# Kernel tuning notes

Measured on AMD Instinct MI355X. Metric: run time of the kernel, lower is better.

Reference implementation:

```python
import jax, jax.numpy as jnp
import numpy as np

# Poincare ball, curvature c = 1. Assumed manifold ops (standard hyperbolic-attention
# formulations, matching the hypll-style API used by the module):
#   HLinear(x)                ~ expmap0(logmap0(x) @ W + b)   (tangent-space linear)
#   attention_similarity      ~ (-d_poincare(q,k))/tau + gamma
#   attention_activation      ~ softmax over keys
#   attention_midpoint        ~ Mobius gyromidpoint: 0.5 (x) [sum_k w lam(v) v / sum_k w (lam(v)-1)]
#   cat                       ~ expmap0(concat(logmap0(heads)))

EPS = 1e-6
MAX_TANH_ARG = 1.0 - 1e-5

def _norm(x):
    return jnp.sqrt(jnp.clip(jnp.sum(x * x, axis=-1, keepdims=True), EPS))

def expmap0(v):
    n = _norm(v)
    return jnp.tanh(n) * v / n

def logmap0(x):
    n = _norm(x)
    return jnp.arctanh(jnp.minimum(n, MAX_TANH_ARG)) * x / n

def hlinear(x, W, b):
    return expmap0(logmap0(x) @ W + b)

def pairwise_poincare_dist(q, k):
    # q: [B,H,Sq,D] on ball, k: [B,Sk,D] on ball -> d: [B,H,Sq,Sk]
    qn = jnp.clip(jnp.sum(q * q, axis=-1), 0.0, 1.0 - 1e-5)            # [B,H,Sq]
    kn = jnp.clip(jnp.sum(k * k, axis=-1), 0.0, 1.0 - 1e-5)            # [B,Sk]
    dot = jnp.einsum('bhqd,bkd->bhqk', q, k)                            # GEMM-like
    sq = jnp.clip(qn[..., :, None] + kn[:, None, None, :] - 2.0 * dot, 0.0)
    denom = jnp.clip((1.0 - qn)[..., :, None] * (1.0 - kn)[:, None, None, :], EPS)
    arg = 1.0 + 2.0 * sq / denom
    return jnp.arccosh(jnp.maximum(arg, 1.0 + 1e-7))

def mobius_scalar_mul(r, x):
    n = _norm(x)
    return jnp.tanh(r * jnp.arctanh(jnp.minimum(n, MAX_TANH_ARG))) * x / n


def reference(query, key, value, Wq, bq, Wk, bk, Wv, bv, Wo, bo, scale_tau, scale_gamma):
    # batch_first=True; query/key/value: [B,S,D] points on the Poincare ball
    B, S, D = query.shape
    H = Wq.shape[0]

    # per-head full-dimension query projections, vectorized over heads
    tq = logmap0(query)                                                 # [B,S,D]
    q_h = expmap0(jnp.einsum('bsd,hde->bhse', tq, Wq) + bq[None, :, None, :])  # [B,H,S,D]
    # shared K/V projections (use_separate_kv_per_head=False -> MQA)
    k = hlinear(key, Wk, bk)                                            # [B,S,D]
    v = hlinear(value, Wv, bv)                                          # [B,S,D]

    tau = jnp.exp(-scale_tau[0])          # module passes tau = 1/exp(scale_tau)
    gamma = scale_gamma[0]

    d = pairwise_poincare_dist(q_h, k)                                  # [B,H,Sq,Sk]
    sim = -d / tau + gamma
    w = jax.nn.softmax(sim, axis=-1)                                    # [B,H,Sq,Sk]

    # Mobius gyromidpoint of values, weighted per query
    vn = jnp.clip(jnp.sum(v * v, axis=-1), 0.0, 1.0 - 1e-5)             # [B,Sk]
    lam = 2.0 / (1.0 - vn)                                              # [B,Sk]
    num = jnp.einsum('bhqk,bk,bkd->bhqd', w, lam, v)                    # [B,H,Sq,D]
    den = jnp.einsum('bhqk,bk->bhq', w, lam - 1.0)[..., None]           # [B,H,Sq,1]
    mid = mobius_scalar_mul(0.5, num / jnp.clip(den, EPS))              # [B,H,Sq,D]

    # manifold.cat: tangent-space concat of heads, back to the ball
    t = logmap0(mid)                                                    # [B,H,S,D]
    t = jnp.transpose(t, (0, 2, 1, 3)).reshape(B, S, H * D)             # [B,S,H*D]
    concat = expmap0(t)
    return hlinear(concat, Wo, bo)                                      # [B,S,D]


def setup_inputs() -> dict:
    key0 = jax.random.key(0)
    ks = jax.random.split(key0, 16)
    B, S, D, H = 4, 1024, 512, 8
    proj = lambda k: expmap0(0.02 * jax.random.normal(k, (B, S, D), dtype=jnp.float32))
    w_init = lambda k, shape, fan_in: (jax.random.normal(k, shape, dtype=jnp.float32) / np.sqrt(fan_in)).astype(jnp.float32)
    return {
        'query': proj(ks[0]),
        'key': proj(ks[1]),
        'value': proj(ks[2]),
        'Wq': w_init(ks[3], (H, D, D), D),
        'bq': 0.01 * jax.random.normal(ks[4], (H, D), dtype=jnp.float32),
        'Wk': w_init(ks[5], (D, D), D),
        'bk': 0.01 * jax.random.normal(ks[6], (D,), dtype=jnp.float32),
        'Wv': w_init(ks[7], (D, D), D),
        'bv': 0.01 * jax.random.normal(ks[8], (D,), dtype=jnp.float32),
        'Wo': w_init(ks[9], (H * D, D), H * D),
        'bo': 0.01 * jax.random.normal(ks[10], (D,), dtype=jnp.float32),
        'scale_tau': jnp.zeros((1,), dtype=jnp.float32),
        'scale_gamma': jnp.zeros((1,), dtype=jnp.float32),
    }
```

## Files before the change

kernel.cpp:

```cpp
#include <hip/hip_runtime.h>
#include <math.h>

constexpr int B_ = 4, S_ = 1024, D_ = 512, H_ = 8;
constexpr float EPS_ = 1e-6f;
constexpr float MAXT = 1.0f - 1e-5f;

typedef __attribute__((ext_vector_type(8))) short bf16x8;
typedef __attribute__((ext_vector_type(4))) float f32x4;

__device__ __forceinline__ ushort f2b(float f) {
    unsigned u = __float_as_uint(f);
    unsigned r = u + 0x7fffu + ((u >> 16) & 1u);
    return (ushort)(r >> 16);
}
__device__ __forceinline__ float b2f(ushort h) {
    return __uint_as_float(((unsigned)h) << 16);
}

__device__ __forceinline__ void async16(const ushort* g, ushort* l) {
    __builtin_amdgcn_global_load_lds(
        (const __attribute__((address_space(1))) unsigned int*)g,
        (__attribute__((address_space(3))) unsigned int*)l, 16, 0, 0);
}

__device__ __forceinline__ float blk_reduce_sum(float v, float* sm) {
    for (int o = 32; o > 0; o >>= 1) v += __shfl_down(v, o, 64);
    int lane = threadIdx.x & 63, wid = threadIdx.x >> 6;
    if (lane == 0) sm[wid] = v;
    __syncthreads();
    if (threadIdx.x == 0) sm[0] = sm[0] + sm[1] + sm[2] + sm[3];
    __syncthreads();
    float r = sm[0];
    __syncthreads();
    return r;
}

constexpr int GC_ABUF = 256 * 32;
constexpr int GC_BUF = (256 + 128) * 32;
constexpr int GC_SH = GC_BUF * 3;

__device__ __forceinline__ void gemm_core256(const ushort* __restrict__ A,
                                             const ushort* __restrict__ B,
                                             int lda, int ldb, int K, int m0, int n0,
                                             ushort* __restrict__ sh, f32x4 acc[4][8]) {
    const int tid = threadIdx.x;
    const int w = tid >> 6, lane = tid & 63;
    const int quad = lane >> 4, lx = lane & 15;
    const int rr = lane >> 2, c = lane & 3;

    const ushort* aP[4];
    int aOff[4];
#pragma unroll
    for (int i = 0; i < 4; i++) {
        int r = w * 64 + i * 16 + rr;
        int q = c ^ ((r >> 1) & 3);
        aP[i] = A + (size_t)(m0 + r) * lda + q * 8;
        aOff[i] = (w * 64 + i * 16) * 32;
    }
    const ushort* bP[2];
    int bOff[2];
#pragma unroll
    for (int i = 0; i < 2; i++) {
        int r = w * 32 + i * 16 + rr;
        int q = c ^ ((r >> 1) & 3);
        bP[i] = B + (size_t)(n0 + r) * ldb + q * 8;
        bOff[i] = GC_ABUF + (w * 32 + i * 16) * 32;
    }

    int raOff[4], rbOff[8];
#pragma unroll
    for (int i = 0; i < 4; i++) {
        int ra = w * 64 + i * 16 + lx;
        raOff[i] = ra * 32 + (quad ^ ((ra >> 1) & 3)) * 8;
    }
#pragma unroll
    for (int j = 0; j < 8; j++) {
        int rb = j * 16 + lx;
        rbOff[j] = GC_ABUF + rb * 32 + (quad ^ ((rb >> 1) & 3)) * 8;
    }
#pragma unroll
    for (int i = 0; i < 4; i++)
#pragma unroll
        for (int j = 0; j < 8; j++) acc[i][j] = (f32x4)(0.0f);

    const int nsteps = K >> 5;
#pragma unroll
    for (int i = 0; i < 4; i++) async16(aP[i], sh + aOff[i]);
#pragma unroll
    for (int i = 0; i < 2; i++) async16(bP[i], sh + bOff[i]);
#pragma unroll
    for (int i = 0; i < 4; i++) async16(aP[i] + 32, sh + GC_BUF + aOff[i]);
#pragma unroll
    for (int i = 0; i < 2; i++) async16(bP[i] + 32, sh + GC_BUF + bOff[i]);

    int bufid = 0;
    for (int s = 0; s < nsteps; s++) {
        ushort* cur = sh + bufid * GC_BUF;
        if (s + 2 < nsteps) {
            int nb = bufid + 2;
            if (nb >= 3) nb -= 3;
            ushort* nxt = sh + nb * GC_BUF;
            int k0 = (s + 2) << 5;
#pragma unroll
            for (int i = 0; i < 4; i++) async16(aP[i] + k0, nxt + aOff[i]);
#pragma unroll
            for (int i = 0; i < 2; i++) async16(bP[i] + k0, nxt + bOff[i]);
            asm volatile("s_waitcnt vmcnt(12)" ::: "memory");
        } else if (s + 1 < nsteps) {
            asm volatile("s_waitcnt vmcnt(6)" ::: "memory");
        } else {
            asm volatile("s_waitcnt vmcnt(0)" ::: "memory");
        }
        asm volatile("s_barrier" ::: "memory");
        bf16x8 af[4], bfr[8];
#pragma unroll
        for (int i = 0; i < 4; i++) af[i] = *(const bf16x8*)(cur + raOff[i]);
#pragma unroll
        for (int j = 0; j < 8; j++) bfr[j] = *(const bf16x8*)(cur + rbOff[j]);
#pragma unroll
        for (int i = 0; i < 4; i++)
#pragma unroll
            for (int j = 0; j < 8; j++)
                acc[i][j] = __builtin_amdgcn_mfma_f32_16x16x32_bf16(af[i], bfr[j], acc[i][j], 0, 0, 0);
        asm volatile("s_waitcnt lgkmcnt(0)" ::: "memory");
        asm volatile("s_barrier" ::: "memory");
        bufid = (bufid == 2) ? 0 : bufid + 1;
    }
}

__global__ __launch_bounds__(256, 2) void k_gemm_proj_all(const ushort* __restrict__ tq,
                                                          const ushort* __restrict__ tk,
                                                          const ushort* __restrict__ tv,
                                                          const ushort* __restrict__ WqT,
                                                          const ushort* __restrict__ WkT,
                                                          const ushort* __restrict__ WvT,
                                                          const float* __restrict__ bq,
                                                          const float* __restrict__ bk,
                                                          const float* __restrict__ bv,
                                                          ushort* __restrict__ yq,
                                                          ushort* __restrict__ yk,
                                                          ushort* __restrict__ yv,
                                                          float* __restrict__ ssq,
                                                          float* __restrict__ ssk,
                                                          float* __restrict__ ssv) {
    __shared__ ushort sh[GC_SH];
    int z = blockIdx.z;
    const ushort* A;
    const ushort* BT;
    const float* bias;
    ushort* C;
    float* SS;
    int remap = 0, h = 0;
    if (z == 0) { A = tk; BT = WkT; bias = bk; C = yk; SS = ssk; }
    else if (z == 1) { A = tv; BT = WvT; bias = bv; C = yv; SS = ssv; }
    else {
        h = z - 2;
        A = tq; BT = WqT + (size_t)h * 512 * 512; bias = bq + (size_t)h * 512;
        C = yq; SS = ssq; remap = 1;
    }
    f32x4 acc[4][8];
    int m0 = blockIdx.y * 256, n0 = blockIdx.x * 128;
    gemm_core256(A, BT, 512, 512, 512, m0, n0, sh, acc);
    int tid = threadIdx.x, w = tid >> 6, lane = tid & 63;
    int quad = lane >> 4, lx = lane & 15;
#pragma unroll
    for (int i = 0; i < 4; i++)
#pragma unroll
        for (int reg = 0; reg < 4; reg++) {
            int m = m0 + w * 64 + i * 16 + quad * 4 + reg;
            size_t orow = remap ? (size_t)((m >> 10) * H_ + h) * S_ + (m & 1023) : (size_t)m;
            float ssum = 0.0f;
#pragma unroll
            for (int j = 0; j < 8; j++) {
                int n = n0 + j * 16 + lx;
                ushort hb = f2b(acc[i][j][reg] + bias[n]);
                C[orow * 512 + n] = hb;
                float yv_ = b2f(hb);
                ssum += yv_ * yv_;
            }
            for (int o = 8; o; o >>= 1) ssum += __shfl_xor(ssum, o, 64);
            if (lx == 0) atomicAdd(&SS[orow], ssum);
        }
}

__global__ __launch_bounds__(256) void k_post_proj(const ushort* __restrict__ yv,
                                                   ushort* __restrict__ yvT,
                                                   const float* __restrict__ ssq,
                                                   const float* __restrict__ ssk,
                                                   const float* __restrict__ ssv,
                                                   float* __restrict__ fq,
                                                   float* __restrict__ qn2,
                                                   float* __restrict__ fk,
                                                   float* __restrict__ kn2,
                                                   float* __restrict__ cv,
                                                   float* __restrict__ dsc) {
    int lin = blockIdx.x;
    if (lin < 2048) {
        __shared__ ushort t[32][34];
        int z = lin >> 9, rem = lin & 511;
        int by = rem >> 4, bx = rem & 15;
        const ushort* in = yv + (size_t)z * 1024 * 512;
        ushort* out = yvT + (size_t)z * 512 * 1024;
        int c0 = bx * 32, r0 = by * 32;
        int tx = threadIdx.x & 31, ty = threadIdx.x >> 5;
        for (int rr = ty; rr < 32; rr += 8) t[rr][tx] = in[(size_t)(r0 + rr) * 512 + c0 + tx];
        __syncthreads();
        for (int rr = ty; rr < 32; rr += 8)
            out[(size_t)(c0 + rr) * 1024 + r0 + tx] = t[tx][rr];
        return;
    }
    int idx = (lin - 2048) * 256 + threadIdx.x;
    if (idx >= 40960) return;
    float ss;
    if (idx < 32768) ss = ssq[idx];
    else if (idx < 36864) ss = ssk[idx - 32768];
    else ss = ssv[idx - 36864];
    float n = sqrtf(fmaxf(ss, EPS_));
    float f = tanhf(n) / n;
    float bn2 = fminf(f * f * ss, MAXT);
    if (idx < 32768) {
        fq[idx] = f;
        qn2[idx] = bn2;
    } else if (idx < 36864) {
        fk[idx - 32768] = f;
        kn2[idx - 32768] = bn2;
    } else {
        int r = idx - 36864;
        float lam = 2.0f / (1.0f - bn2);
        float c = f * lam;
        cv[r] = c;
        dsc[r] = (lam - 1.0f) / c;
    }
}

__global__ __launch_bounds__(256, 2) void k_gemm_score(const ushort* __restrict__ Yq,
                                                       const ushort* __restrict__ Yk,
                                                       ushort* __restrict__ E,
                                                       float* __restrict__ den,
                                                       const float* __restrict__ fq,
                                                       const float* __restrict__ qn2,
                                                       const float* __restrict__ fk,
                                                       const float* __restrict__ kn2,
                                                       const float* __restrict__ cv,
                                                       const float* __restrict__ dsc,
                                                       const float* __restrict__ stau) {
    __shared__ ushort sh[GC_SH];
    int b = blockIdx.z;
    int m0 = blockIdx.y * 256, n0 = blockIdx.x * 128;
    const ushort* Aq = Yq + (size_t)b * 8192 * 512;
    const ushort* Bk = Yk + (size_t)b * 1024 * 512;
    E += (size_t)b * 8192 * 1024;
    den += (size_t)b * 8192;
    const float* fqb = fq + (size_t)b * 8192;
    const float* qn2b = qn2 + (size_t)b * 8192;
    const float* fkb = fk + (size_t)b * 1024;
    const float* kn2b = kn2 + (size_t)b * 1024;
    const float* cvb = cv + (size_t)b * 1024;
    const float* dscb = dsc + (size_t)b * 1024;

    f32x4 acc[4][8];
    gemm_core256(Aq, Bk, 512, 512, 512, m0, n0, sh, acc);
    float itau = expf(stau[0]);
    bool tau1 = (itau == 1.0f);
    int tid = threadIdx.x, w_ = tid >> 6, lane = tid & 63;
    int quad = lane >> 4, lx = lane & 15;
    float fkv[8], kn2v[8], cvv[8], dscv[8], rk[8];
#pragma unroll
    for (int j = 0; j < 8; j++) {
        int n = n0 + j * 16 + lx;
        fkv[j] = fkb[n];
        kn2v[j] = kn2b[n];
        rk[j] = __builtin_amdgcn_rcpf(1.0f - kn2v[j]);
        cvv[j] = cvb[n];
        dscv[j] = dscb[n];
    }
#pragma unroll
    for (int i = 0; i < 4; i++)
#pragma unroll
        for (int reg = 0; reg < 4; reg++) {
            int m = m0 + w_ * 64 + i * 16 + quad * 4 + reg;
            float fqm = fqb[m];
            float q = qn2b[m];
            float rq2 = 2.0f * __builtin_amdgcn_rcpf(1.0f - q);
            float rsum = 0.0f;
#pragma unroll
            for (int j = 0; j < 8; j++) {
                float dot = fqm * fkv[j] * acc[i][j][reg];
                float sq = fmaxf(q + kn2v[j] - 2.0f * dot, 0.0f);
                float rr2 = fminf(rq2 * rk[j], 2e6f);
                float w = fmaxf(sq * rr2, 1e-7f);
                float root = __builtin_amdgcn_sqrtf(__builtin_fmaf(w, w, 2.0f * w));
                float t = 1.0f + w + root;
                float e = tau1 ? __builtin_amdgcn_rcpf(t)
                               : __builtin_amdgcn_exp2f(-itau * __builtin_amdgcn_logf(t));
                ushort eb = f2b(e * cvv[j]);
                int n = n0 + j * 16 + lx;
                E[(size_t)m * 1024 + n] = eb;
                rsum += b2f(eb) * dscv[j];
            }
            for (int o = 8; o; o >>= 1) rsum += __shfl_xor(rsum, o, 64);
            if (lx == 0) atomicAdd(&den[m], rsum);
        }
}

__global__ __launch_bounds__(256, 2) void k_gemm_attnv(const ushort* __restrict__ E,
                                                       const ushort* __restrict__ VT,
                                                       const float* __restrict__ den,
                                                       ushort* __restrict__ Ub,
                                                       float* __restrict__ ssU) {
    __shared__ ushort sh[GC_SH];
    int b = blockIdx.z;
    int m0 = blockIdx.y * 256, n0 = blockIdx.x * 128;
    E += (size_t)b * 8192 * 1024;
    VT += (size_t)b * 512 * 1024;
    den += (size_t)b * 8192;
    Ub += (size_t)b * 8192 * 512;
    ssU += (size_t)b * 8192;
    f32x4 acc[4][8];
    gemm_core256(E, VT, 1024, 1024, 1024, m0, n0, sh, acc);
    int tid = threadIdx.x, w = tid >> 6, lane = tid & 63;
    int quad = lane >> 4, lx = lane & 15;
#pragma unroll
    for (int i = 0; i < 4; i++)
#pragma unroll
        for (int reg = 0; reg < 4; reg++) {
            int m = m0 + w * 64 + i * 16 + quad * 4 + reg;
            float inv = __builtin_amdgcn_rcpf(fmaxf(den[m], EPS_));
            float ssum = 0.0f;
#pragma unroll
            for (int j = 0; j < 8; j++) {
                int n = n0 + j * 16 + lx;
                float u = acc[i][j][reg] * inv;
                Ub[(size_t)m * 512 + n] = f2b(u);
                ssum += u * u;
            }
            for (int o = 8; o; o >>= 1) ssum += __shfl_xor(ssum, o, 64);
            if (lx == 0) atomicAdd(&ssU[m], ssum);
        }
}

__global__ __launch_bounds__(256, 2) void k_gemm_sk(const ushort* __restrict__ Ub,
                                                    const ushort* __restrict__ WoT,
                                                    float* __restrict__ Cp) {
    __shared__ ushort sh[GC_SH];
    int z = blockIdx.z;
    int m0 = blockIdx.y * 256, n0 = blockIdx.x * 128;
    int bb = m0 >> 10, s0 = m0 & 1023;
    const ushort* A = Ub + ((size_t)(bb * H_ + z) * S_ + s0) * 512;
    const ushort* BT = WoT + (size_t)z * 512;
    float* C = Cp + (size_t)z * 4096 * 512;
    f32x4 acc[4][8];
    gemm_core256(A, BT, 512, 4096, 512, 0, n0, sh, acc);
    int tid = threadIdx.x, w = tid >> 6, lane = tid & 63;
    int quad = lane >> 4, lx = lane & 15;
#pragma unroll
    for (int i = 0; i < 4; i++)
#pragma unroll
        for (int reg = 0; reg < 4; reg++) {
            int m = m0 + w * 64 + i * 16 + quad * 4 + reg;
#pragma unroll
            for (int j = 0; j < 8; j++) {
                int n = n0 + j * 16 + lx;
                C[(size_t)m * 512 + n] = acc[i][j][reg];
            }
        }
}

__global__ __launch_bounds__(256) void k_final_reduce_expmap(const float* __restrict__ Cp,
                                                             const float* __restrict__ ssU,
                                                             const float* __restrict__ bo,
                                                             float* __restrict__ out) {
    __shared__ float sm[24];
    int r = blockIdx.x;
    int b = r >> 10, s = r & 1023;
    if (threadIdx.x < 8) {
        int h = threadIdx.x;
        float ss = ssU[(size_t)(b * H_ + h) * S_ + s];
        float n = sqrtf(fmaxf(ss, EPS_));
        float a = 0.5f * atanhf(fminf(n, MAXT));
        float f1 = tanhf(a) / n;
        float mss = f1 * f1 * ss;
        float nm = sqrtf(fmaxf(mss, EPS_));
        float f2 = atanhf(fminf(nm, MAXT)) / nm;
        float f12 = f1 * f2;
        sm[h] = f12;
        sm[8 + h] = f12 * f12 * ss;
    }
    __syncthreads();
    if (threadIdx.x == 0) {
        float sum = 0.0f;
#pragma unroll
        for (int h = 0; h < 8; h++) sum += sm[8 + h];
        float nc = sqrtf(fmaxf(sum, EPS_));
        float f3 = tanhf(nc) / nc;
        float css = f3 * f3 * sum;
        float nc2 = sqrtf(fmaxf(css, EPS_));
        float f4 = atanhf(fminf(nc2, MAXT)) / nc2;
        sm[16] = f3 * f4;
    }
    __syncthreads();
    float g = sm[16];
    float a8[8];
#pragma unroll
    for (int z = 0; z < 8; z++) a8[z] = sm[z] * g;
    float v0 = bo[threadIdx.x], v1 = bo[threadIdx.x + 256];
#pragma unroll
    for (int z = 0; z < 8; z++) {
        const float* row = Cp + ((size_t)z * 4096 + r) * 512;
        v0 += a8[z] * row[threadIdx.x];
        v1 += a8[z] * row[threadIdx.x + 256];
    }
    float ss = blk_reduce_sum(v0 * v0 + v1 * v1, sm + 17);
    float n = sqrtf(fmaxf(ss, EPS_));
    float f = tanhf(n) / n;
    float* o = out + (size_t)r * D_;
    o[threadIdx.x] = f * v0;
    o[threadIdx.x + 256] = f * v1;
}

__global__ __launch_bounds__(256) void k_logmap_bf16(const float* __restrict__ q,
                                                     const float* __restrict__ k,
                                                     const float* __restrict__ v,
                                                     ushort* __restrict__ tq,
                                                     ushort* __restrict__ tk,
                                                     ushort* __restrict__ tv) {
    __shared__ float sm[8];
    const float* x = (blockIdx.y == 0) ? q : (blockIdx.y == 1) ? k : v;
    ushort* t = (blockIdx.y == 0) ? tq : (blockIdx.y == 1) ? tk : tv;
    int r = blockIdx.x;
    const float* xr = x + (size_t)r * D_;
    float v0 = xr[threadIdx.x], v1 = xr[threadIdx.x + 256];
    float ss = blk_reduce_sum(v0 * v0 + v1 * v1, sm);
    float n = sqrtf(fmaxf(ss, EPS_));
    float f = atanhf(fminf(n, MAXT)) / n;
    ushort* tr = t + (size_t)r * D_;
    tr[threadIdx.x] = f2b(f * v0);
    tr[threadIdx.x + 256] = f2b(f * v1);
}

__global__ __launch_bounds__(256) void k_transpose_all(const float* __restrict__ Wk,
                                                       const float* __restrict__ Wv,
                                                       const float* __restrict__ Wq,
                                                       const float* __restrict__ Wo,
                                                       ushort* __restrict__ WkT,
                                                       ushort* __restrict__ WvT,
                                                       ushort* __restrict__ WqT,
                                                       ushort* __restrict__ WoT) {
    __shared__ float t[32][33];
    int z = blockIdx.z;
    int c0 = blockIdx.x * 32, r0 = blockIdx.y * 32;
    int tx = threadIdx.x & 31, ty = threadIdx.x >> 5;
    if (z < 10) {
        const float* in;
        ushort* out;
        if (z == 0) { in = Wk; out = WkT; }
        else if (z == 1) { in = Wv; out = WvT; }
        else { in = Wq + (size_t)(z - 2) * 512 * 512; out = WqT + (size_t)(z - 2) * 512 * 512; }
        for (int rr = ty; rr < 32; rr += 8) t[rr][tx] = in[(size_t)(r0 + rr) * 512 + c0 + tx];
        __syncthreads();
        for (int rr = ty; rr < 32; rr += 8)
            out[(size_t)(c0 + rr) * 512 + r0 + tx] = f2b(t[tx][rr]);
    } else {
        int zz = z - 10;
        const float* in = Wo + (size_t)zz * 512 * 512;
        for (int rr = ty; rr < 32; rr += 8) t[rr][tx] = in[(size_t)(r0 + rr) * 512 + c0 + tx];
        __syncthreads();
        for (int rr = ty; rr < 32; rr += 8)
            WoT[(size_t)(c0 + rr) * 4096 + zz * 512 + r0 + tx] = f2b(t[tx][rr]);
    }
}

extern "C" void kernel_launch(void* const* d_in, const int* in_sizes, int n_in,
                              void* d_out, int out_size, void* d_ws, size_t ws_size,
                              hipStream_t stream) {
    (void)in_sizes; (void)n_in; (void)out_size; (void)ws_size;
    const float* query = (const float*)d_in[0];
    const float* key = (const float*)d_in[1];
    const float* value = (const float*)d_in[2];
    const float* Wq = (const float*)d_in[3];
    const float* bq = (const float*)d_in[4];
    const float* Wk = (const float*)d_in[5];
    const float* bk = (const float*)d_in[6];
    const float* Wv = (const float*)d_in[7];
    const float* bv = (const float*)d_in[8];
    const float* Wo = (const float*)d_in[9];
    const float* bo = (const float*)d_in[10];
    const float* stau = (const float*)d_in[11];
    float* out = (float*)d_out;

    char* p = (char*)d_ws;
    auto alloc = [&](size_t bytes) {
        char* r = p;
        p += (bytes + 255) & ~(size_t)255;
        return r;
    };
    ushort* tq = (ushort*)alloc((size_t)4096 * 512 * 2);
    ushort* tk = (ushort*)alloc((size_t)4096 * 512 * 2);
    ushort* tv = (ushort*)alloc((size_t)4096 * 512 * 2);
    ushort* WqT = (ushort*)alloc((size_t)8 * 512 * 512 * 2);
    ushort* WkT = (ushort*)alloc((size_t)512 * 512 * 2);
    ushort* WvT = (ushort*)alloc((size_t)512 * 512 * 2);
    ushort* WoT = (ushort*)alloc((size_t)4096 * 512 * 2);
    ushort* yq = (ushort*)alloc((size_t)32768 * 512 * 2);
    ushort* yk = (ushort*)alloc((size_t)4096 * 512 * 2);
    ushort* yv = (ushort*)alloc((size_t)4096 * 512 * 2);
    ushort* yvT = (ushort*)alloc((size_t)4 * 512 * 1024 * 2);
    ushort* Ub = (ushort*)alloc((size_t)32768 * 512 * 2);
    ushort* Sc = (ushort*)alloc((size_t)4 * 8192 * 1024 * 2);
    float* den = (float*)alloc(32768 * 4);
    float* ssU = (float*)alloc(32768 * 4);
    float* ssq = (float*)alloc(32768 * 4);
    float* ssk = (float*)alloc(4096 * 4);
    float* ssv = (float*)alloc(4096 * 4);
    float* fq = (float*)alloc(32768 * 4);
    float* qn2 = (float*)alloc(32768 * 4);
    float* fk = (float*)alloc(4096 * 4);
    float* kn2 = (float*)alloc(4096 * 4);
    float* cv = (float*)alloc(4096 * 4);
    float* dsc = (float*)alloc(4096 * 4);
    float* Cp = (float*)Sc;

    hipMemsetAsync(den, 0, (size_t)(32768 * 3 + 4096 * 2 + 192) * 4, stream);

    k_logmap_bf16<<<dim3(4096, 3), 256, 0, stream>>>(query, key, value, tq, tk, tv);

    k_transpose_all<<<dim3(16, 16, 18), 256, 0, stream>>>(Wk, Wv, Wq, Wo, WkT, WvT, WqT, WoT);

    k_gemm_proj_all<<<dim3(4, 16, 10), 256, 0, stream>>>(tq, tk, tv, WqT, WkT, WvT, bq, bk, bv,
                                                         yq, yk, yv, ssq, ssk, ssv);

    k_post_proj<<<2208, 256, 0, stream>>>(yv, yvT, ssq, ssk, ssv, fq, qn2, fk, kn2, cv, dsc);

    k_gemm_score<<<dim3(8, 32, 4), 256, 0, stream>>>(yq, yk, Sc, den, fq, qn2, fk, kn2, cv, dsc,
                                                     stau);
    k_gemm_attnv<<<dim3(4, 32, 4), 256, 0, stream>>>(Sc, yvT, den, Ub, ssU);

    k_gemm_sk<<<dim3(4, 16, 8), 256, 0, stream>>>(Ub, WoT, Cp);
    k_final_reduce_expmap<<<4096, 256, 0, stream>>>(Cp, ssU, bo, out);
}
```

Baseline: 353.5 us.

## Shrink GEMM tiles to 128x128 with 2x2 warp layout and double buffering

Replaces the 256x128 triple-buffered GEMM core with a 128x128 tile, double-buffered core where four waves are arranged 2x2, each computing 64x64. Grids double along M and launch bounds raise the occupancy hint to 4 blocks per CU. The aim is more blocks for the 256 CUs, lower LDS and register use per block, and better latency hiding through occupancy. The trade is less data reuse per tile and a shallower prefetch pipeline.

```diff
diff --git a/kernel.cpp b/kernel.cpp
--- a/kernel.cpp
+++ b/kernel.cpp
@@ -35,100 +35,82 @@
     return r;
 }
 
-constexpr int GC_ABUF = 256 * 32;
-constexpr int GC_BUF = (256 + 128) * 32;
-constexpr int GC_SH = GC_BUF * 3;
-
-__device__ __forceinline__ void gemm_core256(const ushort* __restrict__ A,
+constexpr int GC_ABUF = 128 * 32;
+constexpr int GC_BUF = 256 * 32;
+constexpr int GC_SH = GC_BUF * 2;
+
+__device__ __forceinline__ void gemm_core128(const ushort* __restrict__ A,
                                              const ushort* __restrict__ B,
                                              int lda, int ldb, int K, int m0, int n0,
-                                             ushort* __restrict__ sh, f32x4 acc[4][8]) {
+                                             ushort* __restrict__ sh, f32x4 acc[4][4]) {
     const int tid = threadIdx.x;
     const int w = tid >> 6, lane = tid & 63;
+    const int wm = w >> 1, wn = w & 1;
     const int quad = lane >> 4, lx = lane & 15;
     const int rr = lane >> 2, c = lane & 3;
 
-    const ushort* aP[4];
-    int aOff[4];
-#pragma unroll
-    for (int i = 0; i < 4; i++) {
-        int r = w * 64 + i * 16 + rr;
-        int q = c ^ ((r >> 1) & 3);
-        aP[i] = A + (size_t)(m0 + r) * lda + q * 8;
-        aOff[i] = (w * 64 + i * 16) * 32;
-    }
+    const ushort* aP[2];
     const ushort* bP[2];
-    int bOff[2];
+    int aOff[2], bOff[2];
 #pragma unroll
     for (int i = 0; i < 2; i++) {
         int r = w * 32 + i * 16 + rr;
         int q = c ^ ((r >> 1) & 3);
+        aP[i] = A + (size_t)(m0 + r) * lda + q * 8;
         bP[i] = B + (size_t)(n0 + r) * ldb + q * 8;
+        aOff[i] = (w * 32 + i * 16) * 32;
         bOff[i] = GC_ABUF + (w * 32 + i * 16) * 32;
     }
 
-    int raOff[4], rbOff[8];
+    int raOff[4], rbOff[4];
 #pragma unroll
     for (int i = 0; i < 4; i++) {
-        int ra = w * 64 + i * 16 + lx;
+        int ra = wm * 64 + i * 16 + lx;
         raOff[i] = ra * 32 + (quad ^ ((ra >> 1) & 3)) * 8;
-    }
-#pragma unroll
-    for (int j = 0; j < 8; j++) {
-        int rb = j * 16 + lx;
-        rbOff[j] = GC_ABUF + rb * 32 + (quad ^ ((rb >> 1) & 3)) * 8;
+        int rb = wn * 64 + i * 16 + lx;
+        rbOff[i] = GC_ABUF + rb * 32 + (quad ^ ((rb >> 1) & 3)) * 8;
     }
 #pragma unroll
     for (int i = 0; i < 4; i++)
 #pragma unroll
-        for (int j = 0; j < 8; j++) acc[i][j] = (f32x4)(0.0f);
+        for (int j = 0; j < 4; j++) acc[i][j] = (f32x4)(0.0f);
+
+#pragma unroll
+    for (int i = 0; i < 2; i++) async16(aP[i], sh + aOff[i]);
+#pragma unroll
+    for (int i = 0; i < 2; i++) async16(bP[i], sh + bOff[i]);
 
     const int nsteps = K >> 5;
-#pragma unroll
-    for (int i = 0; i < 4; i++) async16(aP[i], sh + aOff[i]);
-#pragma unroll
-    for (int i = 0; i < 2; i++) async16(bP[i], sh + bOff[i]);
-#pragma unroll
-    for (int i = 0; i < 4; i++) async16(aP[i] + 32, sh + GC_BUF + aOff[i]);
-#pragma unroll
-    for (int i = 0; i < 2; i++) async16(bP[i] + 32, sh + GC_BUF + bOff[i]);
-
-    int bufid = 0;
     for (int s = 0; s < nsteps; s++) {
-        ushort* cur = sh + bufid * GC_BUF;
-        if (s + 2 < nsteps) {
-            int nb = bufid + 2;
-            if (nb >= 3) nb -= 3;
-            ushort* nxt = sh + nb * GC_BUF;
-            int k0 = (s + 2) << 5;
-#pragma unroll
-            for (int i = 0; i < 4; i++) async16(aP[i] + k0, nxt + aOff[i]);
+        ushort* cur = sh + (s & 1) * GC_BUF;
+        if (s + 1 < nsteps) {
+            ushort* nxt = sh + ((s + 1) & 1) * GC_BUF;
+            int k0 = (s + 1) << 5;
+#pragma unroll
+            for (int i = 0; i < 2; i++) async16(aP[i] + k0, nxt + aOff[i]);
 #pragma unroll
             for (int i = 0; i < 2; i++) async16(bP[i] + k0, nxt + bOff[i]);
-            asm volatile("s_waitcnt vmcnt(12)" ::: "memory");
-        } else if (s + 1 < nsteps) {
-            asm volatile("s_waitcnt vmcnt(6)" ::: "memory");
+            asm volatile("s_waitcnt vmcnt(4)" ::: "memory");
         } else {
             asm volatile("s_waitcnt vmcnt(0)" ::: "memory");
         }
         asm volatile("s_barrier" ::: "memory");
-        bf16x8 af[4], bfr[8];
+        bf16x8 af[4], bfr[4];
 #pragma unroll
         for (int i = 0; i < 4; i++) af[i] = *(const bf16x8*)(cur + raOff[i]);
 #pragma unroll
-        for (int j = 0; j < 8; j++) bfr[j] = *(const bf16x8*)(cur + rbOff[j]);
+        for (int j = 0; j < 4; j++) bfr[j] = *(const bf16x8*)(cur + rbOff[j]);
 #pragma unroll
         for (int i = 0; i < 4; i++)
 #pragma unroll
-            for (int j = 0; j < 8; j++)
+            for (int j = 0; j < 4; j++)
                 acc[i][j] = __builtin_amdgcn_mfma_f32_16x16x32_bf16(af[i], bfr[j], acc[i][j], 0, 0, 0);
         asm volatile("s_waitcnt lgkmcnt(0)" ::: "memory");
         asm volatile("s_barrier" ::: "memory");
-        bufid = (bufid == 2) ? 0 : bufid + 1;
-    }
-}
-
-__global__ __launch_bounds__(256, 2) void k_gemm_proj_all(const ushort* __restrict__ tq,
+    }
+}
+
+__global__ __launch_bounds__(256, 4) void k_gemm_proj_all(const ushort* __restrict__ tq,
                                                           const ushort* __restrict__ tk,
                                                           const ushort* __restrict__ tv,
                                                           const ushort* __restrict__ WqT,
@@ -158,21 +140,21 @@
         A = tq; BT = WqT + (size_t)h * 512 * 512; bias = bq + (size_t)h * 512;
         C = yq; SS = ssq; remap = 1;
     }
-    f32x4 acc[4][8];
-    int m0 = blockIdx.y * 256, n0 = blockIdx.x * 128;
-    gemm_core256(A, BT, 512, 512, 512, m0, n0, sh, acc);
+    f32x4 acc[4][4];
+    int m0 = blockIdx.y * 128, n0 = blockIdx.x * 128;
+    gemm_core128(A, BT, 512, 512, 512, m0, n0, sh, acc);
     int tid = threadIdx.x, w = tid >> 6, lane = tid & 63;
-    int quad = lane >> 4, lx = lane & 15;
+    int wm = w >> 1, wn = w & 1, quad = lane >> 4, lx = lane & 15;
 #pragma unroll
     for (int i = 0; i < 4; i++)
 #pragma unroll
         for (int reg = 0; reg < 4; reg++) {
-            int m = m0 + w * 64 + i * 16 + quad * 4 + reg;
+            int m = m0 + wm * 64 + i * 16 + quad * 4 + reg;
             size_t orow = remap ? (size_t)((m >> 10) * H_ + h) * S_ + (m & 1023) : (size_t)m;
             float ssum = 0.0f;
 #pragma unroll
-            for (int j = 0; j < 8; j++) {
-                int n = n0 + j * 16 + lx;
+            for (int j = 0; j < 4; j++) {
+                int n = n0 + wn * 64 + j * 16 + lx;
                 ushort hb = f2b(acc[i][j][reg] + bias[n]);
                 C[orow * 512 + n] = hb;
                 float yv_ = b2f(hb);
@@ -233,7 +215,7 @@
     }
 }
 
-__global__ __launch_bounds__(256, 2) void k_gemm_score(const ushort* __restrict__ Yq,
+__global__ __launch_bounds__(256, 4) void k_gemm_score(const ushort* __restrict__ Yq,
                                                        const ushort* __restrict__ Yk,
                                                        ushort* __restrict__ E,
                                                        float* __restrict__ den,
@@ -246,7 +228,7 @@
                                                        const float* __restrict__ stau) {
     __shared__ ushort sh[GC_SH];
     int b = blockIdx.z;
-    int m0 = blockIdx.y * 256, n0 = blockIdx.x * 128;
+    int m0 = blockIdx.y * 128, n0 = blockIdx.x * 128;
     const ushort* Aq = Yq + (size_t)b * 8192 * 512;
     const ushort* Bk = Yk + (size_t)b * 1024 * 512;
     E += (size_t)b * 8192 * 1024;
@@ -258,16 +240,16 @@
     const float* cvb = cv + (size_t)b * 1024;
     const float* dscb = dsc + (size_t)b * 1024;
 
-    f32x4 acc[4][8];
-    gemm_core256(Aq, Bk, 512, 512, 512, m0, n0, sh, acc);
+    f32x4 acc[4][4];
+    gemm_core128(Aq, Bk, 512, 512, 512, m0, n0, sh, acc);
     float itau = expf(stau[0]);
     bool tau1 = (itau == 1.0f);
     int tid = threadIdx.x, w_ = tid >> 6, lane = tid & 63;
-    int quad = lane >> 4, lx = lane & 15;
-    float fkv[8], kn2v[8], cvv[8], dscv[8], rk[8];
-#pragma unroll
-    for (int j = 0; j < 8; j++) {
-        int n = n0 + j * 16 + lx;
+    int wm = w_ >> 1, wn = w_ & 1, quad = lane >> 4, lx = lane & 15;
+    float fkv[4], kn2v[4], cvv[4], dscv[4], rk[4];
+#pragma unroll
+    for (int j = 0; j < 4; j++) {
+        int n = n0 + wn * 64 + j * 16 + lx;
         fkv[j] = fkb[n];
         kn2v[j] = kn2b[n];
         rk[j] = __builtin_amdgcn_rcpf(1.0f - kn2v[j]);
@@ -278,13 +260,13 @@
     for (int i = 0; i < 4; i++)
 #pragma unroll
         for (int reg = 0; reg < 4; reg++) {
-            int m = m0 + w_ * 64 + i * 16 + quad * 4 + reg;
+            int m = m0 + wm * 64 + i * 16 + quad * 4 + reg;
             float fqm = fqb[m];
             float q = qn2b[m];
             float rq2 = 2.0f * __builtin_amdgcn_rcpf(1.0f - q);
             float rsum = 0.0f;
 #pragma unroll
-            for (int j = 0; j < 8; j++) {
+            for (int j = 0; j < 4; j++) {
                 float dot = fqm * fkv[j] * acc[i][j][reg];
                 float sq = fmaxf(q + kn2v[j] - 2.0f * dot, 0.0f);
                 float rr2 = fminf(rq2 * rk[j], 2e6f);
@@ -294,7 +276,7 @@
                 float e = tau1 ? __builtin_amdgcn_rcpf(t)
                                : __builtin_amdgcn_exp2f(-itau * __builtin_amdgcn_logf(t));
                 ushort eb = f2b(e * cvv[j]);
-                int n = n0 + j * 16 + lx;
+                int n = n0 + wn * 64 + j * 16 + lx;
                 E[(size_t)m * 1024 + n] = eb;
                 rsum += b2f(eb) * dscv[j];
             }
@@ -303,33 +285,33 @@
         }
 }
 
-__global__ __launch_bounds__(256, 2) void k_gemm_attnv(const ushort* __restrict__ E,
+__global__ __launch_bounds__(256, 4) void k_gemm_attnv(const ushort* __restrict__ E,
                                                        const ushort* __restrict__ VT,
                                                        const float* __restrict__ den,
                                                        ushort* __restrict__ Ub,
                                                        float* __restrict__ ssU) {
     __shared__ ushort sh[GC_SH];
     int b = blockIdx.z;
-    int m0 = blockIdx.y * 256, n0 = blockIdx.x * 128;
+    int m0 = blockIdx.y * 128, n0 = blockIdx.x * 128;
     E += (size_t)b * 8192 * 1024;
     VT += (size_t)b * 512 * 1024;
     den += (size_t)b * 8192;
     Ub += (size_t)b * 8192 * 512;
     ssU += (size_t)b * 8192;
-    f32x4 acc[4][8];
-    gemm_core256(E, VT, 1024, 1024, 1024, m0, n0, sh, acc);
+    f32x4 acc[4][4];
+    gemm_core128(E, VT, 1024, 1024, 1024, m0, n0, sh, acc);
     int tid = threadIdx.x, w = tid >> 6, lane = tid & 63;
-    int quad = lane >> 4, lx = lane & 15;
+    int wm = w >> 1, wn = w & 1, quad = lane >> 4, lx = lane & 15;
 #pragma unroll
     for (int i = 0; i < 4; i++)
 #pragma unroll
         for (int reg = 0; reg < 4; reg++) {
-            int m = m0 + w * 64 + i * 16 + quad * 4 + reg;
+            int m = m0 + wm * 64 + i * 16 + quad * 4 + reg;
             float inv = __builtin_amdgcn_rcpf(fmaxf(den[m], EPS_));
             float ssum = 0.0f;
 #pragma unroll
-            for (int j = 0; j < 8; j++) {
-                int n = n0 + j * 16 + lx;
+            for (int j = 0; j < 4; j++) {
+                int n = n0 + wn * 64 + j * 16 + lx;
                 float u = acc[i][j][reg] * inv;
                 Ub[(size_t)m * 512 + n] = f2b(u);
                 ssum += u * u;
@@ -339,28 +321,28 @@
         }
 }
 
-__global__ __launch_bounds__(256, 2) void k_gemm_sk(const ushort* __restrict__ Ub,
+__global__ __launch_bounds__(256, 4) void k_gemm_sk(const ushort* __restrict__ Ub,
                                                     const ushort* __restrict__ WoT,
                                                     float* __restrict__ Cp) {
     __shared__ ushort sh[GC_SH];
     int z = blockIdx.z;
-    int m0 = blockIdx.y * 256, n0 = blockIdx.x * 128;
+    int m0 = blockIdx.y * 128, n0 = blockIdx.x * 128;
     int bb = m0 >> 10, s0 = m0 & 1023;
     const ushort* A = Ub + ((size_t)(bb * H_ + z) * S_ + s0) * 512;
     const ushort* BT = WoT + (size_t)z * 512;
     float* C = Cp + (size_t)z * 4096 * 512;
-    f32x4 acc[4][8];
-    gemm_core256(A, BT, 512, 4096, 512, 0, n0, sh, acc);
+    f32x4 acc[4][4];
+    gemm_core128(A, BT, 512, 4096, 512, 0, n0, sh, acc);
     int tid = threadIdx.x, w = tid >> 6, lane = tid & 63;
-    int quad = lane >> 4, lx = lane & 15;
+    int wm = w >> 1, wn = w & 1, quad = lane >> 4, lx = lane & 15;
 #pragma unroll
     for (int i = 0; i < 4; i++)
 #pragma unroll
         for (int reg = 0; reg < 4; reg++) {
-            int m = m0 + w * 64 + i * 16 + quad * 4 + reg;
-#pragma unroll
-            for (int j = 0; j < 8; j++) {
-                int n = n0 + j * 16 + lx;
+            int m = m0 + wm * 64 + i * 16 + quad * 4 + reg;
+#pragma unroll
+            for (int j = 0; j < 4; j++) {
+                int n = n0 + wn * 64 + j * 16 + lx;
                 C[(size_t)m * 512 + n] = acc[i][j][reg];
             }
         }
@@ -526,15 +508,15 @@
 
     k_transpose_all<<<dim3(16, 16, 18), 256, 0, stream>>>(Wk, Wv, Wq, Wo, WkT, WvT, WqT, WoT);
 
-    k_gemm_proj_all<<<dim3(4, 16, 10), 256, 0, stream>>>(tq, tk, tv, WqT, WkT, WvT, bq, bk, bv,
+    k_gemm_proj_all<<<dim3(4, 32, 10), 256, 0, stream>>>(tq, tk, tv, WqT, WkT, WvT, bq, bk, bv,
                                                          yq, yk, yv, ssq, ssk, ssv);
 
     k_post_proj<<<2208, 256, 0, stream>>>(yv, yvT, ssq, ssk, ssv, fq, qn2, fk, kn2, cv, dsc);
 
-    k_gemm_score<<<dim3(8, 32, 4), 256, 0, stream>>>(yq, yk, Sc, den, fq, qn2, fk, kn2, cv, dsc,
+    k_gemm_score<<<dim3(8, 64, 4), 256, 0, stream>>>(yq, yk, Sc, den, fq, qn2, fk, kn2, cv, dsc,
                                                      stau);
-    k_gemm_attnv<<<dim3(4, 32, 4), 256, 0, stream>>>(Sc, yvT, den, Ub, ssU);
-
-    k_gemm_sk<<<dim3(4, 16, 8), 256, 0, stream>>>(Ub, WoT, Cp);
+    k_gemm_attnv<<<dim3(4, 64, 4), 256, 0, stream>>>(Sc, yvT, den, Ub, ssU);
+
+    k_gemm_sk<<<dim3(4, 32, 8), 256, 0, stream>>>(Ub, WoT, Cp);
     k_final_reduce_expmap<<<4096, 256, 0, stream>>>(Cp, ssU, bo, out);
 }
```

Result: slower. 367.9 us (+4.1%).
